# Kernel tuning notes

Measured on AMD Instinct MI355X. Metric: run time of the kernel, lower is better.

The kernel has to match this reference:

```python
import jax, jax.numpy as jnp
import numpy as np

B, T_H, T_W, S_H, S_W = 64, 8, 8, 20, 20
DIM, HEADS = 768, 12
L = 2 * T_H * T_W + S_H * S_W  # 528


def setup_inputs() -> dict:
    key = jax.random.key(0)
    ks = jax.random.split(key, 6)
    sd = 0.02
    return {
        "x": jax.random.normal(ks[0], (B, L, DIM), jnp.float32),
        "Wq": jax.random.normal(ks[1], (DIM, DIM), jnp.float32) * sd,
        "Wk": jax.random.normal(ks[2], (DIM, DIM), jnp.float32) * sd,
        "Wv": jax.random.normal(ks[3], (DIM, DIM), jnp.float32) * sd,
        "Wp": jax.random.normal(ks[4], (DIM, DIM), jnp.float32) * sd,
        "bp": jnp.zeros((DIM,), jnp.float32),
        "t_h": T_H, "t_w": T_W, "s_h": S_H, "s_w": S_W,
    }


def _heads(y, h):
    b, t, d = y.shape
    return y.reshape(b, t, h, d // h).transpose(0, 2, 1, 3)  # b h t d


def _merge(y):
    b, h, t, d = y.shape
    return y.transpose(0, 2, 1, 3).reshape(b, t, h * d)


def _attn(q, k, v, scale):
    s = jnp.einsum("bhld,bhtd->bhlt", q, k) * scale
    p = jax.nn.softmax(s, axis=-1)
    return jnp.einsum("bhlt,bhtd->bhld", p, v)


def reference(x, Wq, Wk, Wv, Wp, bp, t_h, t_w, s_h, s_w):
    # forward_conv with default path is identity: q = k = v = x
    dim = Wq.shape[1]
    scale = dim ** (-0.5)  # NOTE: full dim_out, faithful to original
    q = _heads(x @ Wq, HEADS)
    k = _heads(x @ Wk, HEADS)
    v = _heads(x @ Wv, HEADS)
    Lt = t_h * t_w
    q_t, q_ot, q_s = q[:, :, :Lt], q[:, :, Lt:2 * Lt], q[:, :, 2 * Lt:]
    k12 = k[:, :, :2 * Lt]  # template+online keys
    v12 = v[:, :, :2 * Lt]
    x_t = _attn(q_t, k12, v12, scale)
    x_ot = _attn(q_ot, k12, v12, scale)
    x_s = _attn(q_s, k, v, scale)  # search attends to everything
    out = jnp.concatenate([_merge(x_t), _merge(x_ot), _merge(x_s)], axis=1)
    return out @ Wp + bp
```

## Files before the change

### kernel.cpp

```cpp
#include <hip/hip_runtime.h>
#include <stdint.h>

typedef __attribute__((ext_vector_type(8))) short bf16x8;
typedef __attribute__((ext_vector_type(4))) float f32x4;
typedef unsigned short ushort_t;
typedef unsigned int u32;
typedef const __attribute__((address_space(1))) u32* gp1_t;
typedef __attribute__((address_space(3))) u32* lp3_t;

#define MFMA(a,b,c) __builtin_amdgcn_mfma_f32_16x16x32_bf16((a),(b),(c),0,0,0)

static constexpr int BATCH = 64, LQ = 528, DIM = 768, NH = 12, DH = 64;
static constexpr int MTOK = BATCH * LQ;
static constexpr int VTP  = 544;
static constexpr float QSCALE = (float)(0.03608439182435161 * 1.4426950408889634);

__device__ __forceinline__ ushort_t f2bf(float f) {
  u32 u = __float_as_uint(f);
  u = (u + 0x7fffu + ((u >> 16) & 1u)) >> 16;
  return (ushort_t)u;
}
__device__ __forceinline__ u32 pack2(u32 xr, u32 yr) {
  return __builtin_amdgcn_perm(xr, yr, 0x07060302u);
}
__device__ __forceinline__ int swzK(int r) { return (r & 3) | (((r >> 3) & 1) << 2); }
__device__ __forceinline__ int swzV(int d) { return (d >> 2) & 3; }

__global__ __launch_bounds__(256) void k_convert_x(const float* __restrict__ x,
                                                   ushort_t* __restrict__ xb) {
  int i = blockIdx.x * 256 + threadIdx.x;
  float4 v = ((const float4*)x)[i];
  ushort4 o;
  o.x = f2bf(v.x); o.y = f2bf(v.y); o.z = f2bf(v.z); o.w = f2bf(v.w);
  ((ushort4*)xb)[i] = o;
}

__global__ __launch_bounds__(256) void k_convert_w(
    const float* __restrict__ w0, const float* __restrict__ w1,
    const float* __restrict__ w2, const float* __restrict__ w3,
    ushort_t* __restrict__ o0, ushort_t* __restrict__ o1,
    ushort_t* __restrict__ o2, ushort_t* __restrict__ o3) {
  __shared__ ushort_t t[64][65];
  int mid = blockIdx.z;
  const float* src = (mid == 0) ? w0 : (mid == 1) ? w1 : (mid == 2) ? w2 : w3;
  ushort_t* dst = (mid == 0) ? o0 : (mid == 1) ? o1 : (mid == 2) ? o2 : o3;
  int k0 = blockIdx.x * 64, n0 = blockIdx.y * 64;
  int c = threadIdx.x & 63, rr = threadIdx.x >> 6;
#pragma unroll
  for (int p = 0; p < 16; p++) {
    int r = p * 4 + rr;
    t[c][r] = f2bf(src[(size_t)(k0 + r) * DIM + n0 + c]);
  }
  __syncthreads();
#pragma unroll
  for (int p = 0; p < 16; p++) {
    int r = p * 4 + rr;
    dst[(size_t)(n0 + r) * DIM + k0 + c] = t[r][c];
  }
}

__global__ __launch_bounds__(256, 2) void k_gemm_qkv(
    const ushort_t* __restrict__ A, const ushort_t* __restrict__ wq,
    const ushort_t* __restrict__ wk, const ushort_t* __restrict__ wv,
    ushort_t* __restrict__ Qb, ushort_t* __restrict__ Kb, ushort_t* __restrict__ Vtb) {
  const int id = blockIdx.x, xcd = id & 7, s = id >> 3;
  const int mT = xcd * 33 + s / 18, t = s % 18, w = t / 6, nT = t % 6;
  const ushort_t* Bt = (w == 0) ? wq : (w == 1) ? wk : wv;

  __shared__ ushort_t at[128 * 64];
  __shared__ ushort_t bt[128 * 64];
  const int tid = threadIdx.x;
  const int wv_ = tid >> 6, lane = tid & 63;
  const int lane15 = lane & 15, quad = lane >> 4;
  const int mw = (wv_ & 1) * 64, nw = (wv_ >> 1) * 64;

  f32x4 acc[4][4];
#pragma unroll
  for (int i = 0; i < 4; i++)
#pragma unroll
    for (int j = 0; j < 4; j++) acc[i][j] = (f32x4)0.0f;

  const int lrow = lane >> 3;
  const int lchunk = lane & 7;

  for (int kb = 0; kb < 768; kb += 64) {
#pragma unroll
    for (int i = 0; i < 4; i++) {
      int r0 = wv_ * 32 + i * 8;
      int lr = r0 + lrow;
      size_t off = (size_t)(mT * 128 + lr) * 768 + kb + ((lchunk ^ (lr & 7)) << 3);
      __builtin_amdgcn_global_load_lds((gp1_t)(A + off), (lp3_t)(&at[r0 * 64]), 16, 0, 0);
    }
#pragma unroll
    for (int i = 0; i < 4; i++) {
      int r0 = wv_ * 32 + i * 8;
      int lr = r0 + lrow;
      size_t off = (size_t)(nT * 128 + lr) * 768 + kb + ((lchunk ^ (lr & 7)) << 3);
      __builtin_amdgcn_global_load_lds((gp1_t)(Bt + off), (lp3_t)(&bt[r0 * 64]), 16, 0, 0);
    }
    __syncthreads();
#pragma unroll
    for (int h = 0; h < 2; h++) {
      bf16x8 af[4], bf[4];
#pragma unroll
      for (int mi = 0; mi < 4; mi++) {
        int row = mw + mi * 16 + lane15;
        af[mi] = *(const bf16x8*)&at[row * 64 + (((h * 4 + quad) ^ (row & 7)) << 3)];
      }
#pragma unroll
      for (int ni = 0; ni < 4; ni++) {
        int row = nw + ni * 16 + lane15;
        bf[ni] = *(const bf16x8*)&bt[row * 64 + (((h * 4 + quad) ^ (row & 7)) << 3)];
      }
#pragma unroll
      for (int mi = 0; mi < 4; mi++)
#pragma unroll
        for (int ni = 0; ni < 4; ni++)
          acc[mi][ni] = MFMA(af[mi], bf[ni], acc[mi][ni]);
    }
    __syncthreads();
  }

  const float scale = (w == 0) ? QSCALE : 1.0f;
  ushort_t* Cqk = (w == 0) ? Qb : Kb;
#pragma unroll
  for (int mi = 0; mi < 4; mi++) {
#pragma unroll
    for (int r = 0; r < 4; r++) {
      int m = mT * 128 + mw + mi * 16 + quad * 4 + r;
      int b = m / 528, lt = m - b * 528;
#pragma unroll
      for (int ni = 0; ni < 4; ni++) {
        int n = nT * 128 + nw + ni * 16 + lane15;
        float v = acc[mi][ni][r];
        if (w < 2) {
          Cqk[(((size_t)(b * 12 + (n >> 6)) * 528 + lt) << 6) + (n & 63)] = f2bf(v * scale);
        } else {
          Vtb[((size_t)(b * 12 + (n >> 6)) * 64 + (n & 63)) * VTP + lt] = f2bf(v);
        }
      }
    }
  }
}

__global__ __launch_bounds__(256, 2) void k_gemm_out(const ushort_t* __restrict__ A,
                                                     const ushort_t* __restrict__ Bt,
                                                     float* __restrict__ C,
                                                     const float* __restrict__ bias) {
  const int id = blockIdx.x, xcd = id & 7, s = id >> 3;
  const int mT = xcd * 33 + s / 6, nT = s % 6;

  __shared__ ushort_t at[128 * 64];
  __shared__ ushort_t bt[128 * 64];
  const int tid = threadIdx.x;
  const int wv_ = tid >> 6, lane = tid & 63;
  const int lane15 = lane & 15, quad = lane >> 4;
  const int mw = (wv_ & 1) * 64, nw = (wv_ >> 1) * 64;

  f32x4 acc[4][4];
#pragma unroll
  for (int i = 0; i < 4; i++)
#pragma unroll
    for (int j = 0; j < 4; j++) acc[i][j] = (f32x4)0.0f;

  const int lrow = lane >> 3;
  const int lchunk = lane & 7;

  for (int kb = 0; kb < 768; kb += 64) {
#pragma unroll
    for (int i = 0; i < 4; i++) {
      int r0 = wv_ * 32 + i * 8;
      int lr = r0 + lrow;
      int grow = mT * 128 + lr;
      int gk = kb + ((lchunk ^ (lr & 7)) << 3);
      int b = grow / 528, ltk = grow - b * 528;
      size_t off = (((size_t)(b * 12 + (gk >> 6)) * 528 + ltk) << 6) + (gk & 63);
      __builtin_amdgcn_global_load_lds((gp1_t)(A + off), (lp3_t)(&at[r0 * 64]), 16, 0, 0);
    }
#pragma unroll
    for (int i = 0; i < 4; i++) {
      int r0 = wv_ * 32 + i * 8;
      int lr = r0 + lrow;
      size_t off = (size_t)(nT * 128 + lr) * 768 + kb + ((lchunk ^ (lr & 7)) << 3);
      __builtin_amdgcn_global_load_lds((gp1_t)(Bt + off), (lp3_t)(&bt[r0 * 64]), 16, 0, 0);
    }
    __syncthreads();
#pragma unroll
    for (int h = 0; h < 2; h++) {
      bf16x8 af[4], bf[4];
#pragma unroll
      for (int mi = 0; mi < 4; mi++) {
        int row = mw + mi * 16 + lane15;
        af[mi] = *(const bf16x8*)&at[row * 64 + (((h * 4 + quad) ^ (row & 7)) << 3)];
      }
#pragma unroll
      for (int ni = 0; ni < 4; ni++) {
        int row = nw + ni * 16 + lane15;
        bf[ni] = *(const bf16x8*)&bt[row * 64 + (((h * 4 + quad) ^ (row & 7)) << 3)];
      }
#pragma unroll
      for (int mi = 0; mi < 4; mi++)
#pragma unroll
        for (int ni = 0; ni < 4; ni++)
          acc[mi][ni] = MFMA(af[mi], bf[ni], acc[mi][ni]);
    }
    __syncthreads();
  }

#pragma unroll
  for (int mi = 0; mi < 4; mi++) {
#pragma unroll
    for (int r = 0; r < 4; r++) {
      int m = mT * 128 + mw + mi * 16 + quad * 4 + r;
#pragma unroll
      for (int ni = 0; ni < 4; ni++) {
        int n = nT * 128 + nw + ni * 16 + lane15;
        C[(size_t)m * 768 + n] = acc[mi][ni][r] + bias[n];
      }
    }
  }
}

__global__ __launch_bounds__(256, 3) void k_attn(ushort_t* __restrict__ Q,
                                                 const ushort_t* __restrict__ K,
                                                 const ushort_t* __restrict__ Vt) {
  __shared__ ushort_t Ksh[2][32 * 64];
  __shared__ ushort_t Vsh[2][64 * 32];
  const int tid = threadIdx.x;
  const int wv = tid >> 6, lane = tid & 63;
  const int lane15 = lane & 15, quad = lane >> 4;
  const int b = blockIdx.x, xcd = b & 7, slot = b >> 3;
  const int g = slot / 17, r = slot - g * 17;
  const int bh0 = (xcd * 24 + g) * 4;

  bf16x8 ones;
#pragma unroll
  for (int i = 0; i < 8; i++) ones[i] = (short)0x3F80;

  const int krp = ((lane15 >> 2) << 3) + (lane15 & 3);

  if (r < 16) {
    const int sub = r & 3;
    const int bh = bh0 + (r >> 2);
    const bool light = (sub == 3);
    const int rows0 = light ? (wv * 32) : (128 + sub * 128 + wv * 32);
    const int nch = light ? 4 : 17;

    ushort_t* Qb = Q + (size_t)bh * LQ * DH;
    const ushort_t* Kbh = K + (size_t)bh * LQ * DH;
    const ushort_t* Vbh = Vt + (size_t)bh * DH * VTP;

    bf16x8 aq[2][2];
#pragma unroll
    for (int mt = 0; mt < 2; mt++)
#pragma unroll
      for (int h = 0; h < 2; h++)
        aq[mt][h] = *(const bf16x8*)&Qb[(size_t)(rows0 + mt * 16 + lane15) * DH + h * 32 + quad * 8];

    f32x4 o[2][4], sm[2];
#pragma unroll
    for (int mt = 0; mt < 2; mt++) {
      sm[mt] = (f32x4)0.0f;
#pragma unroll
      for (int dt = 0; dt < 4; dt++) o[mt][dt] = (f32x4)0.0f;
    }

    auto stageKV = [&](int buf, int kc) {
      {
        int rr = tid >> 3, u = tid & 7;
        const ushort_t* src = Kbh + (size_t)(kc + rr) * DH + ((u ^ swzK(rr)) << 3);
        __builtin_amdgcn_global_load_lds((gp1_t)src, (lp3_t)&Ksh[buf][(wv * 8) * 64], 16, 0, 0);
      }
      {
        int d = tid >> 2, cc = tid & 3;
        const ushort_t* src = Vbh + (size_t)d * VTP + kc + ((cc ^ swzV(d)) << 3);
        __builtin_amdgcn_global_load_lds((gp1_t)src, (lp3_t)&Vsh[buf][(wv * 16) * 32], 16, 0, 0);
      }
    };

    stageKV(0, 0);
    for (int c = 0; c < nch; c++) {
      __syncthreads();
      if (c + 1 < nch) stageKV((c + 1) & 1, (c + 1) * 32);
      const int buf = c & 1;
      bf16x8 kf[2][2], vf[4];
#pragma unroll
      for (int ss = 0; ss < 2; ss++) {
        int kr = krp + ss * 4;
#pragma unroll
        for (int h = 0; h < 2; h++)
          kf[ss][h] = *(const bf16x8*)&Ksh[buf][kr * 64 + (((h * 4 + quad) ^ swzK(kr)) << 3)];
      }
#pragma unroll
      for (int dt = 0; dt < 4; dt++) {
        int d = dt * 16 + lane15;
        vf[dt] = *(const bf16x8*)&Vsh[buf][d * 32 + ((quad ^ swzV(d)) << 3)];
      }
      const bool maskl = (c == 16) && (quad >= 2);
#pragma unroll
      for (int mt = 0; mt < 2; mt++) {
        f32x4 c0 = (f32x4)0.0f, c1 = (f32x4)0.0f;
        c0 = MFMA(kf[0][0], aq[mt][0], c0);
        c0 = MFMA(kf[0][1], aq[mt][1], c0);
        c1 = MFMA(kf[1][0], aq[mt][0], c1);
        c1 = MFMA(kf[1][1], aq[mt][1], c1);
        u32 pw[8];
#pragma unroll
        for (int rr = 0; rr < 4; rr++) {
          float a0 = maskl ? -30.0f : c0[rr];
          float a1 = maskl ? -30.0f : c1[rr];
          pw[rr]     = __float_as_uint(exp2f(a0)) + 0x8000u;
          pw[4 + rr] = __float_as_uint(exp2f(a1)) + 0x8000u;
        }
        union { bf16x8 v; u32 w[4]; } pb;
        pb.w[0] = pack2(pw[1], pw[0]);
        pb.w[1] = pack2(pw[3], pw[2]);
        pb.w[2] = pack2(pw[5], pw[4]);
        pb.w[3] = pack2(pw[7], pw[6]);
        sm[mt] = MFMA(ones, pb.v, sm[mt]);
#pragma unroll
        for (int dt = 0; dt < 4; dt++)
          o[mt][dt] = MFMA(vf[dt], pb.v, o[mt][dt]);
      }
    }

#pragma unroll
    for (int mt = 0; mt < 2; mt++) {
      float inv = 1.0f / sm[mt][0];
      ushort_t* orow = &Qb[(size_t)(rows0 + mt * 16 + lane15) * DH];
#pragma unroll
      for (int dt = 0; dt < 4; dt++) {
        u32 r0 = __float_as_uint(o[mt][dt][0] * inv) + 0x8000u;
        u32 r1 = __float_as_uint(o[mt][dt][1] * inv) + 0x8000u;
        u32 r2 = __float_as_uint(o[mt][dt][2] * inv) + 0x8000u;
        u32 r3 = __float_as_uint(o[mt][dt][3] * inv) + 0x8000u;
        uint2 st;
        st.x = pack2(r1, r0);
        st.y = pack2(r3, r2);
        *(uint2*)&orow[dt * 16 + quad * 4] = st;
      }
    }
  } else {
    const int bh = bh0 + wv;
    ushort_t* Qb = Q + (size_t)bh * LQ * DH;
    const ushort_t* Kbh = K + (size_t)bh * LQ * DH;
    const ushort_t* Vbh = Vt + (size_t)bh * DH * VTP;

    bf16x8 aq[2];
#pragma unroll
    for (int h = 0; h < 2; h++)
      aq[h] = *(const bf16x8*)&Qb[(size_t)(512 + lane15) * DH + h * 32 + quad * 8];

    f32x4 o[4], sm = (f32x4)0.0f;
#pragma unroll
    for (int dt = 0; dt < 4; dt++) o[dt] = (f32x4)0.0f;

    const ushort_t* kbase = Kbh + (size_t)krp * DH + quad * 8;
    const ushort_t* vbase = Vbh + (size_t)lane15 * VTP + quad * 8;

    for (int kc = 0; kc < 528; kc += 32) {
      bf16x8 kf[2][2], vf[4];
#pragma unroll
      for (int ss = 0; ss < 2; ss++) {
        const ushort_t* p = kbase + (size_t)(kc + ss * 4) * DH;
        kf[ss][0] = *(const bf16x8*)&p[0];
        kf[ss][1] = *(const bf16x8*)&p[32];
      }
#pragma unroll
      for (int dt = 0; dt < 4; dt++)
        vf[dt] = *(const bf16x8*)&vbase[(size_t)dt * 16 * VTP + kc];

      f32x4 c0 = (f32x4)0.0f, c1 = (f32x4)0.0f;
      c0 = MFMA(kf[0][0], aq[0], c0);
      c0 = MFMA(kf[0][1], aq[1], c0);
      c1 = MFMA(kf[1][0], aq[0], c1);
      c1 = MFMA(kf[1][1], aq[1], c1);
      const bool maskl = (kc == 512) && (quad >= 2);
      u32 pw[8];
#pragma unroll
      for (int rr = 0; rr < 4; rr++) {
        float a0 = maskl ? -30.0f : c0[rr];
        float a1 = maskl ? -30.0f : c1[rr];
        pw[rr]     = __float_as_uint(exp2f(a0)) + 0x8000u;
        pw[4 + rr] = __float_as_uint(exp2f(a1)) + 0x8000u;
      }
      union { bf16x8 v; u32 w[4]; } pb;
      pb.w[0] = pack2(pw[1], pw[0]);
      pb.w[1] = pack2(pw[3], pw[2]);
      pb.w[2] = pack2(pw[5], pw[4]);
      pb.w[3] = pack2(pw[7], pw[6]);
      sm = MFMA(ones, pb.v, sm);
#pragma unroll
      for (int dt = 0; dt < 4; dt++)
        o[dt] = MFMA(vf[dt], pb.v, o[dt]);
    }

    float inv = 1.0f / sm[0];
    ushort_t* orow = &Qb[(size_t)(512 + lane15) * DH];
#pragma unroll
    for (int dt = 0; dt < 4; dt++) {
      u32 r0 = __float_as_uint(o[dt][0] * inv) + 0x8000u;
      u32 r1 = __float_as_uint(o[dt][1] * inv) + 0x8000u;
      u32 r2 = __float_as_uint(o[dt][2] * inv) + 0x8000u;
      u32 r3 = __float_as_uint(o[dt][3] * inv) + 0x8000u;
      uint2 st;
      st.x = pack2(r1, r0);
      st.y = pack2(r3, r2);
      *(uint2*)&orow[dt * 16 + quad * 4] = st;
    }
  }
}

extern "C" void kernel_launch(void* const* d_in, const int* in_sizes, int n_in,
                              void* d_out, int out_size, void* d_ws, size_t ws_size,
                              hipStream_t stream) {
  const float* x = (const float*)d_in[0];
  const float* Wq = (const float*)d_in[1];
  const float* Wk = (const float*)d_in[2];
  const float* Wv = (const float*)d_in[3];
  const float* Wp = (const float*)d_in[4];
  const float* bp = (const float*)d_in[5];
  float* out = (float*)d_out;

  char* ws = (char*)d_ws;
  size_t off = 0;
  auto alloc = [&](size_t bytes) {
    void* p = ws + off;
    off += (bytes + 255) & ~(size_t)255;
    return p;
  };
  ushort_t* xb = (ushort_t*)alloc((size_t)MTOK * DIM * 2);
  ushort_t* wtq = (ushort_t*)alloc((size_t)DIM * DIM * 2);
  ushort_t* wtk = (ushort_t*)alloc((size_t)DIM * DIM * 2);
  ushort_t* wtv = (ushort_t*)alloc((size_t)DIM * DIM * 2);
  ushort_t* wtp = (ushort_t*)alloc((size_t)DIM * DIM * 2);
  ushort_t* Qb = (ushort_t*)alloc((size_t)MTOK * DIM * 2);
  ushort_t* Kb = (ushort_t*)alloc((size_t)MTOK * DIM * 2);
  ushort_t* Vtb = (ushort_t*)alloc((size_t)BATCH * NH * DH * VTP * 2);
  (void)ws_size; (void)in_sizes; (void)n_in; (void)out_size;

  k_convert_x<<<25344, 256, 0, stream>>>(x, xb);
  k_convert_w<<<dim3(12, 12, 4), 256, 0, stream>>>(Wq, Wk, Wv, Wp, wtq, wtk, wtv, wtp);
  k_gemm_qkv<<<4752, 256, 0, stream>>>(xb, wtq, wtk, wtv, Qb, Kb, Vtb);
  k_attn<<<3264, 256, 0, stream>>>(Qb, Kb, Vtb);
  k_gemm_out<<<1584, 256, 0, stream>>>(Qb, wtp, out, bp);
}
```

Baseline: 515.1 us.

## Enlarge QKV GEMM tiles to 256x256 with double-buffered LDS prefetch

The QKV projection GEMM now uses 512-thread workgroups that each compute a 256x256 output tile, up from 128x128. Global-to-LDS loads for the next K-slice are double-buffered so they overlap the MFMA work on the current slice. The XCD-aware block remap is reworked to assign contiguous tile IDs per XCD, and s_setprio is raised around the MFMA bursts. The goal is more operand reuse per LDS byte and less barrier stall, at the cost of 128KB of LDS per workgroup and higher register pressure that may cut occupancy.

```diff
diff --git a/kernel.cpp b/kernel.cpp
--- a/kernel.cpp
+++ b/kernel.cpp
@@ -59,82 +59,108 @@
   }
 }
 
-__global__ __launch_bounds__(256, 2) void k_gemm_qkv(
+__global__ __launch_bounds__(512, 2) void k_gemm_qkv(
     const ushort_t* __restrict__ A, const ushort_t* __restrict__ wq,
     const ushort_t* __restrict__ wk, const ushort_t* __restrict__ wv,
     ushort_t* __restrict__ Qb, ushort_t* __restrict__ Kb, ushort_t* __restrict__ Vtb) {
-  const int id = blockIdx.x, xcd = id & 7, s = id >> 3;
-  const int mT = xcd * 33 + s / 18, t = s % 18, w = t / 6, nT = t % 6;
+  const int nwg = 1188, qq = nwg >> 3, rmn = nwg & 7;
+  const int orig = blockIdx.x, xcd = orig & 7, within = orig >> 3;
+  const int wgid = (xcd < rmn ? xcd * (qq + 1) : rmn * (qq + 1) + (xcd - rmn) * qq) + within;
+  const int mT = wgid / 9, nT = wgid % 9;
+  const int w = nT / 3, nc0 = (nT % 3) * 256;
   const ushort_t* Bt = (w == 0) ? wq : (w == 1) ? wk : wv;
 
-  __shared__ ushort_t at[128 * 64];
-  __shared__ ushort_t bt[128 * 64];
+  __shared__ ushort_t at[2][256 * 64];
+  __shared__ ushort_t bt[2][256 * 64];
   const int tid = threadIdx.x;
-  const int wv_ = tid >> 6, lane = tid & 63;
+  const int wid = tid >> 6, lane = tid & 63;
   const int lane15 = lane & 15, quad = lane >> 4;
-  const int mw = (wv_ & 1) * 64, nw = (wv_ >> 1) * 64;
-
-  f32x4 acc[4][4];
-#pragma unroll
-  for (int i = 0; i < 4; i++)
+  const int wm = wid >> 2, wn = wid & 3;
+  const int lrow = lane >> 3, lchunk = lane & 7;
+
+  f32x4 acc[8][4];
+#pragma unroll
+  for (int i = 0; i < 8; i++)
 #pragma unroll
     for (int j = 0; j < 4; j++) acc[i][j] = (f32x4)0.0f;
 
-  const int lrow = lane >> 3;
-  const int lchunk = lane & 7;
-
-  for (int kb = 0; kb < 768; kb += 64) {
+  auto stage = [&](int p, int kt) {
+    const int kb = kt * 64;
 #pragma unroll
     for (int i = 0; i < 4; i++) {
-      int r0 = wv_ * 32 + i * 8;
+      int r0 = i * 64 + wid * 8;
       int lr = r0 + lrow;
-      size_t off = (size_t)(mT * 128 + lr) * 768 + kb + ((lchunk ^ (lr & 7)) << 3);
-      __builtin_amdgcn_global_load_lds((gp1_t)(A + off), (lp3_t)(&at[r0 * 64]), 16, 0, 0);
+      size_t off = (size_t)(mT * 256 + lr) * 768 + kb + ((lchunk ^ (lr & 7)) << 3);
+      __builtin_amdgcn_global_load_lds((gp1_t)(A + off), (lp3_t)(&at[p][r0 * 64]), 16, 0, 0);
     }
 #pragma unroll
     for (int i = 0; i < 4; i++) {
-      int r0 = wv_ * 32 + i * 8;
+      int r0 = i * 64 + wid * 8;
       int lr = r0 + lrow;
-      size_t off = (size_t)(nT * 128 + lr) * 768 + kb + ((lchunk ^ (lr & 7)) << 3);
-      __builtin_amdgcn_global_load_lds((gp1_t)(Bt + off), (lp3_t)(&bt[r0 * 64]), 16, 0, 0);
-    }
-    __syncthreads();
-#pragma unroll
-    for (int h = 0; h < 2; h++) {
-      bf16x8 af[4], bf[4];
-#pragma unroll
-      for (int mi = 0; mi < 4; mi++) {
-        int row = mw + mi * 16 + lane15;
-        af[mi] = *(const bf16x8*)&at[row * 64 + (((h * 4 + quad) ^ (row & 7)) << 3)];
-      }
+      size_t off = (size_t)(nc0 + lr) * 768 + kb + ((lchunk ^ (lr & 7)) << 3);
+      __builtin_amdgcn_global_load_lds((gp1_t)(Bt + off), (lp3_t)(&bt[p][r0 * 64]), 16, 0, 0);
+    }
+  };
+
+  stage(0, 0);
+  asm volatile("s_waitcnt vmcnt(0)" ::: "memory");
+  __builtin_amdgcn_s_barrier();
+  __builtin_amdgcn_sched_barrier(0);
+
+  for (int kt = 0; kt < 12; kt++) {
+    const int p = kt & 1;
+    if (kt + 1 < 12) stage(p ^ 1, kt + 1);
+
+    bf16x8 bfr[4][2];
+#pragma unroll
+    for (int ni = 0; ni < 4; ni++)
+#pragma unroll
+      for (int h = 0; h < 2; h++) {
+        int row = wn * 64 + ni * 16 + lane15;
+        bfr[ni][h] = *(const bf16x8*)&bt[p][row * 64 + (((h * 4 + quad) ^ (row & 7)) << 3)];
+      }
+
+#pragma unroll
+    for (int ph = 0; ph < 4; ph++) {
+      bf16x8 af[2][2];
+#pragma unroll
+      for (int m2 = 0; m2 < 2; m2++)
+#pragma unroll
+        for (int h = 0; h < 2; h++) {
+          int row = wm * 128 + (ph * 2 + m2) * 16 + lane15;
+          af[m2][h] = *(const bf16x8*)&at[p][row * 64 + (((h * 4 + quad) ^ (row & 7)) << 3)];
+        }
+      __builtin_amdgcn_s_setprio(1);
+#pragma unroll
+      for (int m2 = 0; m2 < 2; m2++)
+#pragma unroll
+        for (int ni = 0; ni < 4; ni++) {
+          acc[ph * 2 + m2][ni] = MFMA(af[m2][0], bfr[ni][0], acc[ph * 2 + m2][ni]);
+          acc[ph * 2 + m2][ni] = MFMA(af[m2][1], bfr[ni][1], acc[ph * 2 + m2][ni]);
+        }
+      __builtin_amdgcn_s_setprio(0);
+    }
+
+    __builtin_amdgcn_sched_barrier(0);
+    asm volatile("s_waitcnt vmcnt(0)" ::: "memory");
+    __builtin_amdgcn_s_barrier();
+    __builtin_amdgcn_sched_barrier(0);
+  }
+
+  const float scalev = (w == 0) ? QSCALE : 1.0f;
+  ushort_t* Cqk = (w == 0) ? Qb : Kb;
+#pragma unroll
+  for (int mi = 0; mi < 8; mi++) {
+#pragma unroll
+    for (int rr = 0; rr < 4; rr++) {
+      int m = mT * 256 + wm * 128 + mi * 16 + quad * 4 + rr;
+      int b = m / 528, lt = m - b * 528;
 #pragma unroll
       for (int ni = 0; ni < 4; ni++) {
-        int row = nw + ni * 16 + lane15;
-        bf[ni] = *(const bf16x8*)&bt[row * 64 + (((h * 4 + quad) ^ (row & 7)) << 3)];
-      }
-#pragma unroll
-      for (int mi = 0; mi < 4; mi++)
-#pragma unroll
-        for (int ni = 0; ni < 4; ni++)
-          acc[mi][ni] = MFMA(af[mi], bf[ni], acc[mi][ni]);
-    }
-    __syncthreads();
-  }
-
-  const float scale = (w == 0) ? QSCALE : 1.0f;
-  ushort_t* Cqk = (w == 0) ? Qb : Kb;
-#pragma unroll
-  for (int mi = 0; mi < 4; mi++) {
-#pragma unroll
-    for (int r = 0; r < 4; r++) {
-      int m = mT * 128 + mw + mi * 16 + quad * 4 + r;
-      int b = m / 528, lt = m - b * 528;
-#pragma unroll
-      for (int ni = 0; ni < 4; ni++) {
-        int n = nT * 128 + nw + ni * 16 + lane15;
-        float v = acc[mi][ni][r];
+        int n = nc0 + wn * 64 + ni * 16 + lane15;
+        float v = acc[mi][ni][rr];
         if (w < 2) {
-          Cqk[(((size_t)(b * 12 + (n >> 6)) * 528 + lt) << 6) + (n & 63)] = f2bf(v * scale);
+          Cqk[(((size_t)(b * 12 + (n >> 6)) * 528 + lt) << 6) + (n & 63)] = f2bf(v * scalev);
         } else {
           Vtb[((size_t)(b * 12 + (n >> 6)) * 64 + (n & 63)) * VTP + lt] = f2bf(v);
         }
@@ -441,7 +467,7 @@
 
   k_convert_x<<<25344, 256, 0, stream>>>(x, xb);
   k_convert_w<<<dim3(12, 12, 4), 256, 0, stream>>>(Wq, Wk, Wv, Wp, wtq, wtk, wtv, wtp);
-  k_gemm_qkv<<<4752, 256, 0, stream>>>(xb, wtq, wtk, wtv, Qb, Kb, Vtb);
+  k_gemm_qkv<<<1188, 512, 0, stream>>>(xb, wtq, wtk, wtv, Qb, Kb, Vtb);
   k_attn<<<3264, 256, 0, stream>>>(Qb, Kb, Vtb);
   k_gemm_out<<<1584, 256, 0, stream>>>(Qb, wtp, out, bp);
 }
```

Result: slower. 572.6 us (+11.2%).

## Double-buffer LDS tiles in QKV and output GEMMs to overlap loads with MFMA

Applied to the files above, without the earlier changes.

Both projection GEMMs now keep two LDS buffers for the A and B tiles. The next K-slice is issued through global_load_lds into the alternate buffer before the MFMAs on the current buffer run, so global memory latency is hidden behind compute. This doubles LDS use to 64KB per block, which could limit how many blocks fit per CU at launch_bounds(256,2). Correctness depends on the unshown loop-end barrier: the async LDS loads must complete before the next iteration reads them.

```diff
diff --git a/kernel.cpp b/kernel.cpp
--- a/kernel.cpp
+++ b/kernel.cpp
@@ -67,8 +67,8 @@
   const int mT = xcd * 33 + s / 18, t = s % 18, w = t / 6, nT = t % 6;
   const ushort_t* Bt = (w == 0) ? wq : (w == 1) ? wk : wv;
 
-  __shared__ ushort_t at[128 * 64];
-  __shared__ ushort_t bt[128 * 64];
+  __shared__ ushort_t at[2][128 * 64];
+  __shared__ ushort_t bt[2][128 * 64];
   const int tid = threadIdx.x;
   const int wv_ = tid >> 6, lane = tid & 63;
   const int lane15 = lane & 15, quad = lane >> 4;
@@ -83,34 +83,42 @@
   const int lrow = lane >> 3;
   const int lchunk = lane & 7;
 
-  for (int kb = 0; kb < 768; kb += 64) {
+  auto stage = [&](int p, int kb) {
 #pragma unroll
     for (int i = 0; i < 4; i++) {
       int r0 = wv_ * 32 + i * 8;
       int lr = r0 + lrow;
       size_t off = (size_t)(mT * 128 + lr) * 768 + kb + ((lchunk ^ (lr & 7)) << 3);
-      __builtin_amdgcn_global_load_lds((gp1_t)(A + off), (lp3_t)(&at[r0 * 64]), 16, 0, 0);
+      __builtin_amdgcn_global_load_lds((gp1_t)(A + off), (lp3_t)(&at[p][r0 * 64]), 16, 0, 0);
     }
 #pragma unroll
     for (int i = 0; i < 4; i++) {
       int r0 = wv_ * 32 + i * 8;
       int lr = r0 + lrow;
       size_t off = (size_t)(nT * 128 + lr) * 768 + kb + ((lchunk ^ (lr & 7)) << 3);
-      __builtin_amdgcn_global_load_lds((gp1_t)(Bt + off), (lp3_t)(&bt[r0 * 64]), 16, 0, 0);
-    }
-    __syncthreads();
+      __builtin_amdgcn_global_load_lds((gp1_t)(Bt + off), (lp3_t)(&bt[p][r0 * 64]), 16, 0, 0);
+    }
+  };
+
+  stage(0, 0);
+  __syncthreads();
+
+  for (int kt = 0; kt < 12; kt++) {
+    const int p = kt & 1;
+    if (kt < 11) stage(p ^ 1, (kt + 1) * 64);
+    __builtin_amdgcn_sched_barrier(0);
 #pragma unroll
     for (int h = 0; h < 2; h++) {
       bf16x8 af[4], bf[4];
 #pragma unroll
       for (int mi = 0; mi < 4; mi++) {
         int row = mw + mi * 16 + lane15;
-        af[mi] = *(const bf16x8*)&at[row * 64 + (((h * 4 + quad) ^ (row & 7)) << 3)];
+        af[mi] = *(const bf16x8*)&at[p][row * 64 + (((h * 4 + quad) ^ (row & 7)) << 3)];
       }
 #pragma unroll
       for (int ni = 0; ni < 4; ni++) {
         int row = nw + ni * 16 + lane15;
-        bf[ni] = *(const bf16x8*)&bt[row * 64 + (((h * 4 + quad) ^ (row & 7)) << 3)];
+        bf[ni] = *(const bf16x8*)&bt[p][row * 64 + (((h * 4 + quad) ^ (row & 7)) << 3)];
       }
 #pragma unroll
       for (int mi = 0; mi < 4; mi++)
@@ -150,8 +158,8 @@
   const int id = blockIdx.x, xcd = id & 7, s = id >> 3;
   const int mT = xcd * 33 + s / 6, nT = s % 6;
 
-  __shared__ ushort_t at[128 * 64];
-  __shared__ ushort_t bt[128 * 64];
+  __shared__ ushort_t at[2][128 * 64];
+  __shared__ ushort_t bt[2][128 * 64];
   const int tid = threadIdx.x;
   const int wv_ = tid >> 6, lane = tid & 63;
   const int lane15 = lane & 15, quad = lane >> 4;
@@ -166,7 +174,7 @@
   const int lrow = lane >> 3;
   const int lchunk = lane & 7;
 
-  for (int kb = 0; kb < 768; kb += 64) {
+  auto stage = [&](int p, int kb) {
 #pragma unroll
     for (int i = 0; i < 4; i++) {
       int r0 = wv_ * 32 + i * 8;
@@ -175,28 +183,36 @@
       int gk = kb + ((lchunk ^ (lr & 7)) << 3);
       int b = grow / 528, ltk = grow - b * 528;
       size_t off = (((size_t)(b * 12 + (gk >> 6)) * 528 + ltk) << 6) + (gk & 63);
-      __builtin_amdgcn_global_load_lds((gp1_t)(A + off), (lp3_t)(&at[r0 * 64]), 16, 0, 0);
+      __builtin_amdgcn_global_load_lds((gp1_t)(A + off), (lp3_t)(&at[p][r0 * 64]), 16, 0, 0);
     }
 #pragma unroll
     for (int i = 0; i < 4; i++) {
       int r0 = wv_ * 32 + i * 8;
       int lr = r0 + lrow;
       size_t off = (size_t)(nT * 128 + lr) * 768 + kb + ((lchunk ^ (lr & 7)) << 3);
-      __builtin_amdgcn_global_load_lds((gp1_t)(Bt + off), (lp3_t)(&bt[r0 * 64]), 16, 0, 0);
-    }
-    __syncthreads();
+      __builtin_amdgcn_global_load_lds((gp1_t)(Bt + off), (lp3_t)(&bt[p][r0 * 64]), 16, 0, 0);
+    }
+  };
+
+  stage(0, 0);
+  __syncthreads();
+
+  for (int kt = 0; kt < 12; kt++) {
+    const int p = kt & 1;
+    if (kt < 11) stage(p ^ 1, (kt + 1) * 64);
+    __builtin_amdgcn_sched_barrier(0);
 #pragma unroll
     for (int h = 0; h < 2; h++) {
       bf16x8 af[4], bf[4];
 #pragma unroll
       for (int mi = 0; mi < 4; mi++) {
         int row = mw + mi * 16 + lane15;
-        af[mi] = *(const bf16x8*)&at[row * 64 + (((h * 4 + quad) ^ (row & 7)) << 3)];
+        af[mi] = *(const bf16x8*)&at[p][row * 64 + (((h * 4 + quad) ^ (row & 7)) << 3)];
       }
 #pragma unroll
       for (int ni = 0; ni < 4; ni++) {
         int row = nw + ni * 16 + lane15;
-        bf[ni] = *(const bf16x8*)&bt[row * 64 + (((h * 4 + quad) ^ (row & 7)) << 3)];
+        bf[ni] = *(const bf16x8*)&bt[p][row * 64 + (((h * 4 + quad) ^ (row & 7)) << 3)];
       }
 #pragma unroll
       for (int mi = 0; mi < 4; mi++)
```

After: 520.1 us. Within noise of the previous version (+1.0%).
